# Kernel optimization log

Hardware: AMD Instinct MI355X
Metric: run time of the kernel (lower is better)

The kernel has to match this reference:

```python
import jax, jax.numpy as jnp
import numpy as np

B, N, C, H, W = 4, 3, 128, 128, 128
NH, NP, NL, WS, CT = 4, 4, 3, 8, 64
HD = C // NH
GROUPS = 8
DT_GAIN, MOS, EPS = 1.0, 1.5, 1e-5


def conv1x1(x, w, b):
    return jnp.einsum('bchw,oc->bohw', x, w) + b[None, :, None, None]


def group_norm(x, gamma, beta):
    b, c, h, w = x.shape
    xg = x.reshape(b, GROUPS, -1)
    mu = xg.mean(-1, keepdims=True)
    var = xg.var(-1, keepdims=True)
    xn = ((xg - mu) * jax.lax.rsqrt(var + EPS)).reshape(b, c, h, w)
    return xn * gamma[None, :, None, None] + beta[None, :, None, None]


def window_partition(x):
    b, c, h, w = x.shape
    hw, ww = h // WS, w // WS
    x = x.reshape(b, c, hw, WS, ww, WS).transpose(0, 2, 4, 1, 3, 5)
    return x.reshape(b * hw * ww, c, WS, WS)


def window_reverse(win, hw, ww, b):
    c = win.shape[1]
    x = win.reshape(b, hw, ww, c, WS, WS).transpose(0, 3, 1, 4, 2, 5)
    return x.reshape(b, c, hw * WS, ww * WS)


def bilinear_sample(v_flat, xy):
    # v_flat: [N,BW,NH,WS*WS,HD]; xy in [-1,1]: [BW,WS,WS,NH,NL,NP,2]
    # torch grid_sample, align_corners=False, padding_mode='border'
    ix = jnp.clip(((xy[..., 0] + 1.0) * WS - 1.0) * 0.5, 0.0, WS - 1.0)
    iy = jnp.clip(((xy[..., 1] + 1.0) * WS - 1.0) * 0.5, 0.0, WS - 1.0)
    x0 = jnp.floor(ix)
    y0 = jnp.floor(iy)
    wx = ix - x0
    wy = iy - y0
    x0i = x0.astype(jnp.int32)
    y0i = y0.astype(jnp.int32)
    x1i = jnp.minimum(x0i + 1, WS - 1)
    y1i = jnp.minimum(y0i + 1, WS - 1)

    def to_nbh(a):  # [BW,WS,WS,NH,NL,NP] -> [NL,BW,NH,WS*WS*NP]
        return jnp.transpose(a, (4, 0, 3, 1, 2, 5)).reshape(a.shape[4], a.shape[0], a.shape[3], -1)

    def gather(yi, xi):
        idx = to_nbh(yi * WS + xi)
        return jnp.take_along_axis(v_flat, idx[..., None], axis=3)

    wxt = to_nbh(wx)[..., None]
    wyt = to_nbh(wy)[..., None]
    top = gather(y0i, x0i) * (1.0 - wxt) + gather(y0i, x1i) * wxt
    bot = gather(y1i, x0i) * (1.0 - wxt) + gather(y1i, x1i) * wxt
    return top * (1.0 - wyt) + bot * wyt  # [NL,BW,NH,WS*WS*NP,HD]


def _forward(query, values, rel_scalar, tgt_enc, so1_w, so1_b, gno_g, gno_b,
             so2_w, so2_b, aw1_w, aw1_b, gna_g, gna_b, aw2_w, aw2_b,
             vproj_w, vproj_b, oproj_w, oproj_b, filmo_w, filmo_b,
             filma_w, filma_b, dts_w, dts_b, level_embed,
             conf1_w, conf1_b, conf2_w, conf2_b):
    Bq, Cq, Hq, Wq = query.shape
    hw, ww = Hq // WS, Wq // WS
    num_win = hw * ww
    BW = Bq * num_win
    q_win = window_partition(query)                        # [BW,C,ws,ws]
    v_all = jax.vmap(window_partition, in_axes=1)(values)  # [N,BW,C,ws,ws]

    film_o = jnp.tile(tgt_enc @ filmo_w.T + filmo_b, (num_win, 1))[:, :, None, None]
    film_a = jnp.tile(tgt_enc @ filma_w.T + filma_b, (num_win, 1))[:, :, None, None]

    offsets = conv1x1(jax.nn.relu(group_norm(conv1x1(q_win + film_o, so1_w, so1_b), gno_g, gno_b)), so2_w, so2_b)
    attn_raw = conv1x1(jax.nn.relu(group_norm(conv1x1(q_win + film_a, aw1_w, aw1_b), gna_g, gna_b)), aw2_w, aw2_b)

    attn6 = attn_raw.reshape(BW, NH, NL, NP, WS, WS).transpose(0, 4, 5, 1, 2, 3)  # [BW,ws,ws,NH,NL,NP]
    dt = rel_scalar[:, :N]
    dt_bw = jnp.tile(dt, (num_win, 1))
    bias6 = -DT_GAIN * jnp.abs(dt_bw)[:, None, None, None, :, None]
    attn = jax.nn.softmax((attn6 + bias6).reshape(BW, WS, WS, NH, NL * NP), axis=-1)
    attn6s = attn.reshape(BW, WS, WS, NH, NL, NP)

    probs = attn + 1e-8
    ent = -(probs * jnp.log(probs)).sum(-1).mean(-1)  # [BW,ws,ws]

    lin = jnp.linspace(0.0, 1.0, WS)
    yg, xg = jnp.meshgrid(lin, lin, indexing='ij')
    ref = jnp.stack([xg, yg], -1)  # [ws,ws,2]
    off = offsets.reshape(BW, NH, NL, NP, 2, WS, WS).transpose(0, 5, 6, 1, 2, 3, 4)
    xy = jnp.clip(ref[None, :, :, None, None, None, :] + off, 0.0, 1.0) * 2.0 - 1.0

    hscale = 1.0 + (MOS - 1.0) * jax.nn.sigmoid(jnp.abs(dt)[..., None] * dts_w[:, 0] + dts_b)  # [B,N,NH]
    hscale_bw = jnp.repeat(hscale, num_win, axis=0)
    xy = jnp.clip(xy * jnp.transpose(hscale_bw, (0, 2, 1))[:, None, None, :, :, None, None], -1.0, 1.0)

    v_proj = (jnp.einsum('nbchw,oc->nbohw', v_all + level_embed[:, None, :, None, None], vproj_w)
              + vproj_b[None, None, :, None, None])
    v_flat = v_proj.reshape(N, BW, NH, HD, WS * WS).transpose(0, 1, 2, 4, 3)  # [N,BW,NH,ws*ws,HD]

    sampled = bilinear_sample(v_flat, xy).reshape(N, BW, NH, WS, WS, NP, HD)
    out = jnp.einsum('nbhijpd,bijhnp->bhdij', sampled, attn6s).reshape(BW, C, WS, WS)

    fused = window_reverse(conv1x1(out, oproj_w, oproj_b), hw, ww, Bq)
    c1 = jax.lax.conv_general_dilated(fused, conf1_w, (1, 1), ((1, 1), (1, 1)),
                                      dimension_numbers=('NCHW', 'OIHW', 'NCHW')) + conf1_b[None, :, None, None]
    conf = jax.nn.sigmoid(conv1x1(jax.nn.relu(c1), conf2_w, conf2_b))
    entropy = window_reverse(ent[:, None], hw, ww, Bq)
    return fused, conf, entropy


def setup_inputs() -> dict:
    ks = jax.random.split(jax.random.key(0), 32)

    def nrm(i, shape, s=0.05):
        return jax.random.normal(ks[i], shape, jnp.float32) * s

    return dict(
        query=jax.random.normal(ks[0], (B, C, H, W), jnp.float32),
        values=jax.random.normal(ks[1], (B, N, C, H, W), jnp.float32),
        rel_scalar=jax.random.normal(ks[2], (B, N), jnp.float32),
        tgt_enc=jax.random.normal(ks[3], (B, CT), jnp.float32),
        so1_w=nrm(4, (C // 2, C)), so1_b=nrm(5, (C // 2,)),
        gno_g=jnp.ones((C // 2,), jnp.float32), gno_b=jnp.zeros((C // 2,), jnp.float32),
        so2_w=nrm(6, (NH * NL * NP * 2, C // 2)), so2_b=nrm(7, (NH * NL * NP * 2,)),
        aw1_w=nrm(8, (C // 2, C)), aw1_b=nrm(9, (C // 2,)),
        gna_g=jnp.ones((C // 2,), jnp.float32), gna_b=jnp.zeros((C // 2,), jnp.float32),
        aw2_w=nrm(10, (NH * NL * NP, C // 2)), aw2_b=nrm(11, (NH * NL * NP,)),
        vproj_w=nrm(12, (C, C)), vproj_b=nrm(13, (C,)),
        oproj_w=nrm(14, (C, C)), oproj_b=nrm(15, (C,)),
        filmo_w=nrm(16, (C, CT)), filmo_b=nrm(17, (C,)),
        filma_w=nrm(18, (C, CT)), filma_b=nrm(19, (C,)),
        dts_w=nrm(20, (NH, 1)), dts_b=nrm(21, (NH,)),
        level_embed=nrm(22, (NL, C), 0.02),
        conf1_w=nrm(23, (C // 4, C, 3, 3)), conf1_b=nrm(24, (C // 4,)),
        conf2_w=nrm(25, (1, C // 4)), conf2_b=nrm(26, (1,)),
    )


def reference(query, values, rel_scalar, tgt_enc, so1_w, so1_b, gno_g, gno_b,
              so2_w, so2_b, aw1_w, aw1_b, gna_g, gna_b, aw2_w, aw2_b,
              vproj_w, vproj_b, oproj_w, oproj_b, filmo_w, filmo_b,
              filma_w, filma_b, dts_w, dts_b, level_embed,
              conf1_w, conf1_b, conf2_w, conf2_b):
    return _forward(query, values, rel_scalar, tgt_enc, so1_w, so1_b, gno_g, gno_b,
                    so2_w, so2_b, aw1_w, aw1_b, gna_g, gna_b, aw2_w, aw2_b,
                    vproj_w, vproj_b, oproj_w, oproj_b, filmo_w, filmo_b,
                    filma_w, filma_b, dts_w, dts_b, level_embed,
                    conf1_w, conf1_b, conf2_w, conf2_b)
```

## Files before the change

kernel.cpp:

```cpp
#include <hip/hip_runtime.h>
#include <math.h>

#define NB 4
#define NVAL 3
#define NC 128
#define NHW 128
#define NHEAD 4
#define NPOINT 4
#define NLVL 3
#define WSZ 8
#define HD 32
#define NWIN 256
#define BWTOT 1024
#define NPIX 64

#define WS_SO1BA 0
#define WS_AW1BA 256
#define WS_VB    512
#define WS_HS    896
#define WS_ABSDT 944
#define WT_VP    1024
#define WT_OP    17408
#define WT_SO1   33792
#define WT_AW1   41984
#define WT_SO2   50176
#define WT_AW2   56320
#define WT_C1    59392
#define WS_COORD 96256
#define WS_ATTN  (96256 + 6291456)
#define WS_VFLAT (96256 + 6291456 + 3145728)

#define OUT_FUSED 0
#define OUT_CONF  8388608
#define OUT_ENT   (8388608 + 65536)

__device__ __forceinline__ int ufl(int x) { return __builtin_amdgcn_readfirstlane(x); }

__global__ __launch_bounds__(256) void prep_kernel(
    const float* __restrict__ tgt_enc, const float* __restrict__ filmo_w, const float* __restrict__ filmo_b,
    const float* __restrict__ filma_w, const float* __restrict__ filma_b,
    const float* __restrict__ so1_w, const float* __restrict__ so1_b,
    const float* __restrict__ aw1_w, const float* __restrict__ aw1_b,
    const float* __restrict__ so2_w, const float* __restrict__ aw2_w,
    const float* __restrict__ vproj_w, const float* __restrict__ vproj_b,
    const float* __restrict__ oproj_w, const float* __restrict__ conf1_w,
    const float* __restrict__ level_embed,
    const float* __restrict__ rel_scalar, const float* __restrict__ dts_w, const float* __restrict__ dts_b,
    float* __restrict__ ws)
{
    int tid = threadIdx.x;
    if (blockIdx.x == 0) {
        __shared__ float film[1024];
        for (int t = tid; t < 1024; t += 256) {
            int which = t >> 9; int b = (t >> 7) & 3; int c = t & 127;
            const float* fw = which ? filma_w : filmo_w;
            const float* fb = which ? filma_b : filmo_b;
            float acc = fb[c];
            for (int k = 0; k < 64; ++k) acc += tgt_enc[b * 64 + k] * fw[c * 64 + k];
            film[t] = acc;
        }
        __syncthreads();
        for (int t = tid; t < 512; t += 256) {
            int which = t >> 8; int fb = (t >> 6) & 3; int o = t & 63;
            const float* w  = which ? aw1_w : so1_w;
            const float* bb = which ? aw1_b : so1_b;
            const float* fm = &film[which * 512 + fb * 128];
            float acc = bb[o];
            for (int c = 0; c < 128; ++c) acc += w[o * 128 + c] * fm[c];
            ws[(which ? WS_AW1BA : WS_SO1BA) + fb * 64 + o] = acc;
        }
        for (int t = tid; t < 384; t += 256) {
            int n = t >> 7; int o = t & 127;
            float acc = vproj_b[o];
            for (int c = 0; c < 128; ++c) acc += level_embed[n * 128 + c] * vproj_w[o * 128 + c];
            ws[WS_VB + t] = acc;
        }
        if (tid < 48) {
            int b = tid / 12; int n = (tid / 4) % 3; int hh = tid & 3;
            float ad = fabsf(rel_scalar[b * 3 + n]);
            float s = 1.0f / (1.0f + expf(-(ad * dts_w[hh] + dts_b[hh])));
            ws[WS_HS + tid] = 1.0f + 0.5f * s;
        }
        if (tid < 12) ws[WS_ABSDT + tid] = fabsf(rel_scalar[tid]);
    } else {
        int base = (blockIdx.x - 1) * 256 + tid;
        {
            int c = base >> 7, o = base & 127;
            ws[WT_VP + base] = vproj_w[o * 128 + c];
            ws[WT_OP + base] = oproj_w[o * 128 + c];
        }
        if (base < 8192) {
            int c = base >> 6, o = base & 63;
            ws[WT_SO1 + base] = so1_w[o * 128 + c];
            ws[WT_AW1 + base] = aw1_w[o * 128 + c];
        }
        if (base < 6144) {
            int c = base / 96, o = base - c * 96;
            ws[WT_SO2 + base] = so2_w[o * 64 + c];
        }
        if (base < 3072) {
            int c = base / 48, o = base - c * 48;
            ws[WT_AW2 + base] = aw2_w[o * 64 + c];
        }
        for (int t = base; t < 36864; t += 16384) {
            int c = t / 288; int rem = t - c * 288; int k = rem / 9, tap = rem - k * 9;
            ws[WT_C1 + t] = conf1_w[(k * 128 + c) * 9 + tap];
        }
    }
}

__global__ __launch_bounds__(256) void win_kernel(
    const float* __restrict__ query,
    const float* __restrict__ so2_b,
    const float* __restrict__ gno_g, const float* __restrict__ gno_b,
    const float* __restrict__ aw2_b,
    const float* __restrict__ gna_g, const float* __restrict__ gna_b,
    float* __restrict__ ws, float* __restrict__ out)
{
    __shared__ float sA[8192];
    __shared__ float sYso[4096];
    __shared__ float sYaw[4096];

    int tid = threadIdx.x;
    int bw  = blockIdx.x;
    int b   = bw >> 8;
    int win = bw & 255;
    int wy = win >> 4, wx = win & 15;
    int fb = bw & 3;
    int pix = tid & 63;
    int og  = ufl(tid >> 6);

    const float* qbase = query + ((size_t)b << 21);
    for (int idx = tid; idx < 2048; idx += 256) {
        int c = idx >> 4, j = idx & 15;
        int row = j >> 1, half = j & 1;
        int gh = wy * 8 + row, gw0 = wx * 8 + half * 4;
        const float4 v = *(const float4*)(qbase + (c << 14) + (gh << 7) + gw0);
        *(float4*)(&sA[(c << 6) + (row << 3) + half * 4]) = v;
    }
    __syncthreads();

    {
        float accs[16], acca[16];
#pragma unroll
        for (int k = 0; k < 16; ++k) { accs[k] = 0.f; acca[k] = 0.f; }
#pragma unroll 4
        for (int c = 0; c < 128; ++c) {
            float q = sA[(c << 6) + pix];
            const float* ws1 = ws + WT_SO1 + c * 64 + og * 16;
            const float* wa1 = ws + WT_AW1 + c * 64 + og * 16;
#pragma unroll
            for (int k = 0; k < 16; ++k) {
                accs[k] += ws1[k] * q;
                acca[k] += wa1[k] * q;
            }
        }
        const float* ba_s = ws + WS_SO1BA + fb * 64;
        const float* ba_a = ws + WS_AW1BA + fb * 64;
#pragma unroll
        for (int k = 0; k < 16; ++k) {
            int o = og * 16 + k;
            sYso[(o << 6) + pix] = accs[k] + ba_s[o];
            sYaw[(o << 6) + pix] = acca[k] + ba_a[o];
        }
    }
    __syncthreads();

    {
        float s = 0.f, sq = 0.f;
        int base = tid * 16;
#pragma unroll
        for (int k = 0; k < 16; ++k) { float v = sYso[base + k]; s += v; sq += v * v; }
        sA[tid] = s; sA[256 + tid] = sq;
    }
    __syncthreads();
    if (tid < 8) {
        float s = 0.f, sq = 0.f;
        for (int k = 0; k < 32; ++k) { s += sA[tid * 32 + k]; sq += sA[256 + tid * 32 + k]; }
        float mu = s * (1.f / 512.f);
        float var = sq * (1.f / 512.f) - mu * mu;
        sA[512 + tid] = mu;
        sA[520 + tid] = 1.f / sqrtf(var + 1e-5f);
    }
    __syncthreads();
    {
        int base = tid * 16;
        int g = tid >> 5;
        int c = tid >> 2;
        float mu = sA[512 + g], rs = sA[520 + g];
        float ga = gno_g[c], be = gno_b[c];
#pragma unroll
        for (int k = 0; k < 16; ++k) {
            float v = (sYso[base + k] - mu) * rs * ga + be;
            sYso[base + k] = fmaxf(v, 0.f);
        }
    }
    __syncthreads();

    {
        float acc[24];
#pragma unroll
        for (int k = 0; k < 24; ++k) acc[k] = 0.f;
#pragma unroll 4
        for (int c = 0; c < 64; ++c) {
            float y = sYso[(c << 6) + pix];
            const float* w = ws + WT_SO2 + c * 96 + og * 24;
#pragma unroll
            for (int k = 0; k < 24; ++k) acc[k] += w[k] * y;
        }
#pragma unroll
        for (int k = 0; k < 24; ++k) {
            int ch = og * 24 + k;
            sA[1024 + (ch << 6) + pix] = acc[k] + so2_b[ch];
        }
    }
    __syncthreads();

    {
        int hh = og;
        int btrue = bw >> 8;
        float refx = (float)(pix & 7) * (1.f / 7.f);
        float refy = (float)(pix >> 3) * (1.f / 7.f);
        float* co = ws + WS_COORD + ((((size_t)bw * 64 + pix) * 4 + hh) * 24);
#pragma unroll
        for (int l = 0; l < 3; ++l) {
            float hs = ws[WS_HS + (btrue * 3 + l) * 4 + hh];
#pragma unroll
            for (int p = 0; p < 4; ++p) {
                int chx = ((hh * 3 + l) * 4 + p) * 2;
                float ox = sA[1024 + (chx << 6) + pix];
                float oy = sA[1024 + ((chx + 1) << 6) + pix];
                float x = fminf(fmaxf(refx + ox, 0.f), 1.f) * 2.f - 1.f;
                float y = fminf(fmaxf(refy + oy, 0.f), 1.f) * 2.f - 1.f;
                x = fminf(fmaxf(x * hs, -1.f), 1.f);
                y = fminf(fmaxf(y * hs, -1.f), 1.f);
                float ix = fminf(fmaxf(((x + 1.f) * 8.f - 1.f) * 0.5f, 0.f), 7.f);
                float iy = fminf(fmaxf(((y + 1.f) * 8.f - 1.f) * 0.5f, 0.f), 7.f);
                co[(l * 4 + p) * 2]     = ix;
                co[(l * 4 + p) * 2 + 1] = iy;
            }
        }
    }
    {
        float s = 0.f, sq = 0.f;
        int base = tid * 16;
#pragma unroll
        for (int k = 0; k < 16; ++k) { float v = sYaw[base + k]; s += v; sq += v * v; }
        sA[tid] = s; sA[256 + tid] = sq;
    }
    __syncthreads();
    if (tid < 8) {
        float s = 0.f, sq = 0.f;
        for (int k = 0; k < 32; ++k) { s += sA[tid * 32 + k]; sq += sA[256 + tid * 32 + k]; }
        float mu = s * (1.f / 512.f);
        float var = sq * (1.f / 512.f) - mu * mu;
        sA[512 + tid] = mu;
        sA[520 + tid] = 1.f / sqrtf(var + 1e-5f);
    }
    __syncthreads();
    {
        int base = tid * 16;
        int g = tid >> 5;
        int c = tid >> 2;
        float mu = sA[512 + g], rs = sA[520 + g];
        float ga = gna_g[c], be = gna_b[c];
#pragma unroll
        for (int k = 0; k < 16; ++k) {
            float v = (sYaw[base + k] - mu) * rs * ga + be;
            sYaw[base + k] = fmaxf(v, 0.f);
        }
    }
    __syncthreads();

    {
        float acc[12];
#pragma unroll
        for (int k = 0; k < 12; ++k) acc[k] = 0.f;
#pragma unroll 4
        for (int c = 0; c < 64; ++c) {
            float y = sYaw[(c << 6) + pix];
            const float* w = ws + WT_AW2 + c * 48 + og * 12;
#pragma unroll
            for (int k = 0; k < 12; ++k) acc[k] += w[k] * y;
        }
        __syncthreads();
#pragma unroll
        for (int k = 0; k < 12; ++k) {
            int ch = og * 12 + k;
            sA[1024 + (ch << 6) + pix] = acc[k] + aw2_b[ch];
        }
    }
    __syncthreads();

    {
        int hh = og;
        const float* ad = ws + WS_ABSDT + fb * 3;
        float lg[12];
        float m = -1e30f;
#pragma unroll
        for (int q = 0; q < 12; ++q) {
            float v = sA[1024 + (((hh * 12 + q)) << 6) + pix] - ad[q >> 2];
            lg[q] = v; m = fmaxf(m, v);
        }
        float sum = 0.f;
#pragma unroll
        for (int q = 0; q < 12; ++q) { lg[q] = expf(lg[q] - m); sum += lg[q]; }
        float inv = 1.f / sum;
        float* at = ws + WS_ATTN + ((((size_t)bw * 64 + pix) * 4 + hh) * 12);
        float hent = 0.f;
#pragma unroll
        for (int q = 0; q < 12; ++q) {
            float p = lg[q] * inv;
            at[q] = p;
            float pp = p + 1e-8f;
            hent -= pp * logf(pp);
        }
        sA[pix * 4 + hh] = hent;
    }
    __syncthreads();
    if (tid < 64) {
        float e = 0.25f * (sA[tid * 4] + sA[tid * 4 + 1] + sA[tid * 4 + 2] + sA[tid * 4 + 3]);
        int gh = wy * 8 + (tid >> 3), gw = wx * 8 + (tid & 7);
        out[OUT_ENT + (b << 14) + (gh << 7) + gw] = e;
    }
}

__global__ __launch_bounds__(256) void vproj_kernel(
    const float* __restrict__ values, float* __restrict__ ws)
{
    __shared__ float sbuf[8448];
    int tid = threadIdx.x;
    int bid = blockIdx.x;
    int n = bid >> 10;
    int bw = bid & 1023;
    int b = bw >> 8; int win = bw & 255;
    int wy = win >> 4, wx = win & 15;
    const float* vbase = values + ((size_t)(b * 3 + n) << 21);
    for (int idx = tid; idx < 2048; idx += 256) {
        int c = idx >> 4, j = idx & 15;
        int row = j >> 1, half = j & 1;
        int gh = wy * 8 + row, gw0 = wx * 8 + half * 4;
        const float4 v = *(const float4*)(vbase + (c << 14) + (gh << 7) + gw0);
        *(float4*)(&sbuf[(c << 6) + (row << 3) + half * 4]) = v;
    }
    int pix = tid & 63;
    int og = ufl(tid >> 6);
    float vbr[32];
    {
        const float* vb = ws + WS_VB + n * 128 + og * 32;
#pragma unroll
        for (int k = 0; k < 32; ++k) vbr[k] = vb[k];
    }
    __syncthreads();
    float acc[32];
#pragma unroll
    for (int k = 0; k < 32; ++k) acc[k] = 0.f;
#pragma unroll 4
    for (int c = 0; c < 128; ++c) {
        float v = sbuf[(c << 6) + pix];
        const float* w = ws + WT_VP + c * 128 + og * 32;
#pragma unroll
        for (int k = 0; k < 32; ++k) acc[k] += w[k] * v;
    }
    __syncthreads();
    int row = (og << 6) + pix;
#pragma unroll
    for (int k = 0; k < 32; ++k) sbuf[row * 33 + k] = acc[k] + vbr[k];
    __syncthreads();
    float* base2 = ws + WS_VFLAT + ((((size_t)n << 10) + bw) << 13);
#pragma unroll
    for (int i = 0; i < 8; ++i) {
        int f4 = (i * 256 + tid) * 4;
        int r = f4 >> 5, k = f4 & 31;
        float4 v = make_float4(sbuf[r * 33 + k], sbuf[r * 33 + k + 1],
                               sbuf[r * 33 + k + 2], sbuf[r * 33 + k + 3]);
        *(float4*)(base2 + f4) = v;
    }
}

__global__ __launch_bounds__(256, 4) void sample_kernel(
    const float* __restrict__ oproj_b,
    float* __restrict__ ws, float* __restrict__ out)
{
    __shared__ float smem[9216];
    int tid = threadIdx.x;
    int bw = blockIdx.x;
    int b = bw >> 8; int win = bw & 255;
    int wy = win >> 4, wx = win & 15;
    int pix = tid & 63;
    int hh = ufl(tid >> 6);

    const float* co = ws + WS_COORD + ((size_t)(bw * 64 + pix) * 4 + hh) * 24;
    const float* at = ws + WS_ATTN  + ((size_t)(bw * 64 + pix) * 4 + hh) * 12;

    float acc[32];
#pragma unroll
    for (int k = 0; k < 32; ++k) acc[k] = 0.f;

    for (int l = 0; l < 3; ++l) {
        float4 cxy0 = *(const float4*)(co + l * 8);
        float4 cxy1 = *(const float4*)(co + l * 8 + 4);
        float4 a4   = *(const float4*)(at + l * 4);
        if (l) __syncthreads();
        const float* vsrc = ws + WS_VFLAT + ((((size_t)l << 10) + bw) << 13);
        for (int i = tid; i < 2048; i += 256) {
            float4 v = *(const float4*)(vsrc + i * 4);
            int r = i >> 3, c4 = (i & 7) << 2;
            *(float4*)(&smem[r * 36 + c4]) = v;
        }
        __syncthreads();

        const float* vb = &smem[hh * (64 * 36)];
        float ixs[4] = {cxy0.x, cxy0.z, cxy1.x, cxy1.z};
        float iys[4] = {cxy0.y, cxy0.w, cxy1.y, cxy1.w};
        float as4[4] = {a4.x, a4.y, a4.z, a4.w};
#pragma unroll
        for (int p = 0; p < 4; ++p) {
            float ix = ixs[p], iy = iys[p], a = as4[p];
            float x0f = floorf(ix), y0f = floorf(iy);
            int x0 = (int)x0f, y0 = (int)y0f;
            float wxf = ix - x0f, wyf = iy - y0f;
            int x1 = x0 + 1; if (x1 > 7) x1 = 7;
            int y1 = y0 + 1; if (y1 > 7) y1 = 7;
            float w00 = a * (1.f - wxf) * (1.f - wyf);
            float w01 = a * wxf * (1.f - wyf);
            float w10 = a * (1.f - wxf) * wyf;
            float w11 = a * wxf * wyf;
            const float* r00 = vb + ((y0 << 3) + x0) * 36;
            const float* r01 = vb + ((y0 << 3) + x1) * 36;
            const float* r10 = vb + ((y1 << 3) + x0) * 36;
            const float* r11 = vb + ((y1 << 3) + x1) * 36;
#pragma unroll
            for (int ch = 0; ch < 8; ++ch) {
                float4 v00 = *(const float4*)(r00 + (ch << 2));
                float4 v01 = *(const float4*)(r01 + (ch << 2));
                float4 v10 = *(const float4*)(r10 + (ch << 2));
                float4 v11 = *(const float4*)(r11 + (ch << 2));
                acc[(ch << 2) + 0] += w00 * v00.x + w01 * v01.x + w10 * v10.x + w11 * v11.x;
                acc[(ch << 2) + 1] += w00 * v00.y + w01 * v01.y + w10 * v10.y + w11 * v11.y;
                acc[(ch << 2) + 2] += w00 * v00.z + w01 * v01.z + w10 * v10.z + w11 * v11.z;
                acc[(ch << 2) + 3] += w00 * v00.w + w01 * v01.w + w10 * v10.w + w11 * v11.w;
            }
        }
    }
    __syncthreads();
#pragma unroll
    for (int k = 0; k < 32; ++k)
        smem[(hh * 32 + k) * 65 + pix] = acc[k];
    __syncthreads();

    float acc2[32];
#pragma unroll
    for (int k = 0; k < 32; ++k) acc2[k] = 0.f;
#pragma unroll 4
    for (int c = 0; c < 128; ++c) {
        float v = smem[c * 65 + pix];
        const float* w = ws + WT_OP + c * 128 + hh * 32;
#pragma unroll
        for (int k = 0; k < 32; ++k) acc2[k] += w[k] * v;
    }
    int gh = wy * 8 + (pix >> 3), gw = wx * 8 + (pix & 7);
#pragma unroll
    for (int k = 0; k < 32; ++k) {
        int o = hh * 32 + k;
        out[OUT_FUSED + ((size_t)(b * 128 + o) << 14) + (gh << 7) + gw] = acc2[k] + oproj_b[o];
    }
}

__global__ __launch_bounds__(256) void conf_kernel(
    const float* __restrict__ fused, const float* __restrict__ conf1_b,
    const float* __restrict__ conf2_w, const float* __restrict__ conf2_b,
    const float* __restrict__ ws, float* __restrict__ out)
{
    __shared__ float tile[64 * 110];
    __shared__ float red[4][64];
    int tid = threadIdx.x;
    int bid = blockIdx.x;
    int b = bid >> 8;
    int t = bid & 255; int ty = t >> 4, tx = t & 15;
    int pix = tid & 63;
    int kg  = ufl(tid >> 6);
    int py = pix >> 3, px = pix & 7;
    int oy = ty * 8, ox = tx * 8;
    const float* fin = fused + ((size_t)b << 21);

    float acc[8];
#pragma unroll
    for (int j = 0; j < 8; ++j) acc[j] = 0.f;

    for (int cc = 0; cc < 2; ++cc) {
        __syncthreads();
        for (int idx = tid; idx < 6400; idx += 256) {
            int c = idx / 100;
            int rem = idx - c * 100;
            int r = rem / 10, col = rem - r * 10;
            int gy = oy + r - 1, gx = ox + col - 1;
            float v = 0.f;
            if (gy >= 0 && gy < 128 && gx >= 0 && gx < 128)
                v = fin[((size_t)(cc * 64 + c) << 14) + (gy << 7) + gx];
            tile[c * 110 + r * 11 + col] = v;
        }
        __syncthreads();
        for (int c = 0; c < 64; ++c) {
            float v[9];
#pragma unroll
            for (int dy = 0; dy < 3; ++dy)
#pragma unroll
                for (int dx = 0; dx < 3; ++dx)
                    v[dy * 3 + dx] = tile[c * 110 + (py + dy) * 11 + (px + dx)];
            const float* wp = ws + WT_C1 + ufl((cc * 64 + c) * 288 + kg * 72);
#pragma unroll
            for (int j = 0; j < 8; ++j) {
#pragma unroll
                for (int tap = 0; tap < 9; ++tap)
                    acc[j] += v[tap] * wp[j * 9 + tap];
            }
        }
    }
    float s = 0.f;
#pragma unroll
    for (int j = 0; j < 8; ++j) {
        int k = kg * 8 + j;
        s += fmaxf(acc[j] + conf1_b[k], 0.f) * conf2_w[k];
    }
    red[kg][pix] = s;
    __syncthreads();
    if (tid < 64) {
        float tot = red[0][tid] + red[1][tid] + red[2][tid] + red[3][tid] + conf2_b[0];
        float cf = 1.f / (1.f + expf(-tot));
        int gy = oy + (tid >> 3), gx = ox + (tid & 7);
        out[OUT_CONF + (b << 14) + (gy << 7) + gx] = cf;
    }
}

extern "C" void kernel_launch(void* const* d_in, const int* in_sizes, int n_in,
                              void* d_out, int out_size, void* d_ws, size_t ws_size,
                              hipStream_t stream) {
    const float* query      = (const float*)d_in[0];
    const float* values     = (const float*)d_in[1];
    const float* rel_scalar = (const float*)d_in[2];
    const float* tgt_enc    = (const float*)d_in[3];
    const float* so1_w = (const float*)d_in[4];
    const float* so1_b = (const float*)d_in[5];
    const float* gno_g = (const float*)d_in[6];
    const float* gno_b = (const float*)d_in[7];
    const float* so2_w = (const float*)d_in[8];
    const float* so2_b = (const float*)d_in[9];
    const float* aw1_w = (const float*)d_in[10];
    const float* aw1_b = (const float*)d_in[11];
    const float* gna_g = (const float*)d_in[12];
    const float* gna_b = (const float*)d_in[13];
    const float* aw2_w = (const float*)d_in[14];
    const float* aw2_b = (const float*)d_in[15];
    const float* vproj_w = (const float*)d_in[16];
    const float* vproj_b = (const float*)d_in[17];
    const float* oproj_w = (const float*)d_in[18];
    const float* oproj_b = (const float*)d_in[19];
    const float* filmo_w = (const float*)d_in[20];
    const float* filmo_b = (const float*)d_in[21];
    const float* filma_w = (const float*)d_in[22];
    const float* filma_b = (const float*)d_in[23];
    const float* dts_w   = (const float*)d_in[24];
    const float* dts_b   = (const float*)d_in[25];
    const float* level_embed = (const float*)d_in[26];
    const float* conf1_w = (const float*)d_in[27];
    const float* conf1_b = (const float*)d_in[28];
    const float* conf2_w = (const float*)d_in[29];
    const float* conf2_b = (const float*)d_in[30];

    float* ws  = (float*)d_ws;
    float* out = (float*)d_out;

    prep_kernel<<<65, 256, 0, stream>>>(tgt_enc, filmo_w, filmo_b, filma_w, filma_b,
                                        so1_w, so1_b, aw1_w, aw1_b,
                                        so2_w, aw2_w,
                                        vproj_w, vproj_b, oproj_w, conf1_w,
                                        level_embed, rel_scalar, dts_w, dts_b, ws);
    win_kernel<<<BWTOT, 256, 0, stream>>>(query, so2_b, gno_g, gno_b,
                                          aw2_b, gna_g, gna_b, ws, out);
    vproj_kernel<<<NVAL * BWTOT, 256, 0, stream>>>(values, ws);
    sample_kernel<<<BWTOT, 256, 0, stream>>>(oproj_b, ws, out);
    conf_kernel<<<NB * 256, 256, 0, stream>>>(out, conf1_b, conf2_w, conf2_b, ws, out);
}
```

Measured before the change: 659.7 us.

## Fuse value projection into sampling kernel to drop VFLAT round-trip

Removes the separate vproj kernel and computes the per-window value projection inside sample_kernel, loading raw values into shared memory and projecting per level before bilinear sampling. This eliminates writing and rereading the projected value buffer in global memory (about 100MB of traffic) and one launch. In exchange sample_kernel uses more shared memory and registers, the launch bound drops to 2 blocks per SM, and the projection work now runs inside a 1024-block grid instead of a 3072-block grid.

Result: slower. 879.6 us (+33.3%).

```diff
diff --git a/kernel.cpp b/kernel.cpp
--- a/kernel.cpp
+++ b/kernel.cpp
@@ -28,7 +28,6 @@
 #define WT_C1    59392
 #define WS_COORD 96256
 #define WS_ATTN  (96256 + 6291456)
-#define WS_VFLAT (96256 + 6291456 + 3145728)
 
 #define OUT_FUSED 0
 #define OUT_CONF  8388608
@@ -325,64 +324,12 @@
     }
 }
 
-__global__ __launch_bounds__(256) void vproj_kernel(
-    const float* __restrict__ values, float* __restrict__ ws)
-{
-    __shared__ float sbuf[8448];
-    int tid = threadIdx.x;
-    int bid = blockIdx.x;
-    int n = bid >> 10;
-    int bw = bid & 1023;
-    int b = bw >> 8; int win = bw & 255;
-    int wy = win >> 4, wx = win & 15;
-    const float* vbase = values + ((size_t)(b * 3 + n) << 21);
-    for (int idx = tid; idx < 2048; idx += 256) {
-        int c = idx >> 4, j = idx & 15;
-        int row = j >> 1, half = j & 1;
-        int gh = wy * 8 + row, gw0 = wx * 8 + half * 4;
-        const float4 v = *(const float4*)(vbase + (c << 14) + (gh << 7) + gw0);
-        *(float4*)(&sbuf[(c << 6) + (row << 3) + half * 4]) = v;
-    }
-    int pix = tid & 63;
-    int og = ufl(tid >> 6);
-    float vbr[32];
-    {
-        const float* vb = ws + WS_VB + n * 128 + og * 32;
-#pragma unroll
-        for (int k = 0; k < 32; ++k) vbr[k] = vb[k];
-    }
-    __syncthreads();
-    float acc[32];
-#pragma unroll
-    for (int k = 0; k < 32; ++k) acc[k] = 0.f;
-#pragma unroll 4
-    for (int c = 0; c < 128; ++c) {
-        float v = sbuf[(c << 6) + pix];
-        const float* w = ws + WT_VP + c * 128 + og * 32;
-#pragma unroll
-        for (int k = 0; k < 32; ++k) acc[k] += w[k] * v;
-    }
-    __syncthreads();
-    int row = (og << 6) + pix;
-#pragma unroll
-    for (int k = 0; k < 32; ++k) sbuf[row * 33 + k] = acc[k] + vbr[k];
-    __syncthreads();
-    float* base2 = ws + WS_VFLAT + ((((size_t)n << 10) + bw) << 13);
-#pragma unroll
-    for (int i = 0; i < 8; ++i) {
-        int f4 = (i * 256 + tid) * 4;
-        int r = f4 >> 5, k = f4 & 31;
-        float4 v = make_float4(sbuf[r * 33 + k], sbuf[r * 33 + k + 1],
-                               sbuf[r * 33 + k + 2], sbuf[r * 33 + k + 3]);
-        *(float4*)(base2 + f4) = v;
-    }
-}
-
-__global__ __launch_bounds__(256, 4) void sample_kernel(
-    const float* __restrict__ oproj_b,
+__global__ __launch_bounds__(256, 2) void sample_kernel(
+    const float* __restrict__ values, const float* __restrict__ oproj_b,
     float* __restrict__ ws, float* __restrict__ out)
 {
-    __shared__ float smem[9216];
+    __shared__ float bufA[8448];
+    __shared__ float bufB[9216];
     int tid = threadIdx.x;
     int bw = blockIdx.x;
     int b = bw >> 8; int win = bw & 255;
@@ -401,16 +348,40 @@
         float4 cxy0 = *(const float4*)(co + l * 8);
         float4 cxy1 = *(const float4*)(co + l * 8 + 4);
         float4 a4   = *(const float4*)(at + l * 4);
+
         if (l) __syncthreads();
-        const float* vsrc = ws + WS_VFLAT + ((((size_t)l << 10) + bw) << 13);
-        for (int i = tid; i < 2048; i += 256) {
-            float4 v = *(const float4*)(vsrc + i * 4);
-            int r = i >> 3, c4 = (i & 7) << 2;
-            *(float4*)(&smem[r * 36 + c4]) = v;
+        const float* vbase = values + ((size_t)(b * 3 + l) << 21);
+        for (int idx = tid; idx < 2048; idx += 256) {
+            int c = idx >> 4, j = idx & 15;
+            int row = j >> 1, half = j & 1;
+            int gh = wy * 8 + row, gw0 = wx * 8 + half * 4;
+            const float4 v = *(const float4*)(vbase + (c << 14) + (gh << 7) + gw0);
+            *(float4*)(&bufA[(c << 6) + (row << 3) + half * 4]) = v;
         }
         __syncthreads();
 
-        const float* vb = &smem[hh * (64 * 36)];
+        float vp[32];
+        {
+            const float* vb0 = ws + WS_VB + l * 128 + hh * 32;
+#pragma unroll
+            for (int k = 0; k < 32; ++k) vp[k] = vb0[k];
+        }
+#pragma unroll 4
+        for (int c = 0; c < 128; ++c) {
+            float v = bufA[(c << 6) + pix];
+            const float* w = ws + WT_VP + c * 128 + hh * 32;
+#pragma unroll
+            for (int k = 0; k < 32; ++k) vp[k] += w[k] * v;
+        }
+        {
+            float* dst = &bufB[hh * 2304 + pix * 36];
+#pragma unroll
+            for (int k = 0; k < 32; k += 4)
+                *(float4*)(dst + k) = make_float4(vp[k], vp[k + 1], vp[k + 2], vp[k + 3]);
+        }
+        __syncthreads();
+
+        const float* vb = &bufB[hh * 2304];
         float ixs[4] = {cxy0.x, cxy0.z, cxy1.x, cxy1.z};
         float iys[4] = {cxy0.y, cxy0.w, cxy1.y, cxy1.w};
         float as4[4] = {a4.x, a4.y, a4.z, a4.w};
@@ -446,7 +417,7 @@
     __syncthreads();
 #pragma unroll
     for (int k = 0; k < 32; ++k)
-        smem[(hh * 32 + k) * 65 + pix] = acc[k];
+        bufA[(hh * 32 + k) * 65 + pix] = acc[k];
     __syncthreads();
 
     float acc2[32];
@@ -454,7 +425,7 @@
     for (int k = 0; k < 32; ++k) acc2[k] = 0.f;
 #pragma unroll 4
     for (int c = 0; c < 128; ++c) {
-        float v = smem[c * 65 + pix];
+        float v = bufA[c * 65 + pix];
         const float* w = ws + WT_OP + c * 128 + hh * 32;
 #pragma unroll
         for (int k = 0; k < 32; ++k) acc2[k] += w[k] * v;
@@ -578,7 +549,6 @@
                                         level_embed, rel_scalar, dts_w, dts_b, ws);
     win_kernel<<<BWTOT, 256, 0, stream>>>(query, so2_b, gno_g, gno_b,
                                           aw2_b, gna_g, gna_b, ws, out);
-    vproj_kernel<<<NVAL * BWTOT, 256, 0, stream>>>(values, ws);
-    sample_kernel<<<BWTOT, 256, 0, stream>>>(oproj_b, ws, out);
+    sample_kernel<<<BWTOT, 256, 0, stream>>>(values, oproj_b, ws, out);
     conf_kernel<<<NB * 256, 256, 0, stream>>>(out, conf1_b, conf2_w, conf2_b, ws, out);
 }
```
